# Kernel optimization log

Hardware: AMD Instinct MI355X
Metric: run time of the kernel (lower is better)

Reference implementation:

```python
import jax, jax.numpy as jnp
import numpy as np

D = 384      # embedding_dim
H = 6        # num_heads
HD = D // H  # head_dim = 64
S = 256      # seq_len
B = 64       # batch
EPS = 1e-5


def setup_inputs() -> dict:
    key = jax.random.key(0)
    ks = jax.random.split(key, 16)
    scale = 0.02
    inp = {
        'x': jax.random.normal(ks[0], (B, S, D), dtype=jnp.float32),
        'wq': jax.random.normal(ks[1], (D, D), dtype=jnp.float32) * scale,
        'wk': jax.random.normal(ks[2], (D, D), dtype=jnp.float32) * scale,
        'wv': jax.random.normal(ks[3], (D, D), dtype=jnp.float32) * scale,
        'wo': jax.random.normal(ks[4], (D, D), dtype=jnp.float32) * scale,
        'bo': jnp.zeros((D,), dtype=jnp.float32),
        'w1': jax.random.normal(ks[5], (D, 4 * D), dtype=jnp.float32) * scale,
        'b1': jnp.zeros((4 * D,), dtype=jnp.float32),
        'w2': jax.random.normal(ks[6], (4 * D, D), dtype=jnp.float32) * scale,
        'b2': jnp.zeros((D,), dtype=jnp.float32),
        'g1': jnp.ones((D,), dtype=jnp.float32),
        'be1': jnp.zeros((D,), dtype=jnp.float32),
        'g2': jnp.ones((D,), dtype=jnp.float32),
        'be2': jnp.zeros((D,), dtype=jnp.float32),
    }
    return inp


def _layernorm(x, g, b):
    m = jnp.mean(x, axis=-1, keepdims=True)
    v = jnp.mean((x - m) ** 2, axis=-1, keepdims=True)
    return (x - m) * jax.lax.rsqrt(v + EPS) * g + b


def _block(x, wq, wk, wv, wo, bo, w1, b1, w2, b2, g1, be1, g2, be2):
    b, s, d = x.shape
    h = _layernorm(x, g1, be1)
    # batched per-head projections (equivalent to 6 separate small Linears concatenated)
    q = (h @ wq).reshape(b, s, H, HD).transpose(0, 2, 1, 3)  # [B,H,S,HD]
    k = (h @ wk).reshape(b, s, H, HD).transpose(0, 2, 1, 3)
    v = (h @ wv).reshape(b, s, H, HD).transpose(0, 2, 1, 3)
    scores = jnp.einsum('bhqe,bhke->bhqk', q, k) / np.float32(np.sqrt(HD))
    causal = jnp.tril(jnp.ones((s, s), dtype=bool))
    scores = jnp.where(causal, scores, -jnp.inf)
    attn = jax.nn.softmax(scores, axis=-1)  # dropout = identity in eval
    ctx = jnp.einsum('bhqk,bhke->bhqe', attn, v)  # [B,H,S,HD]
    ctx = ctx.transpose(0, 2, 1, 3).reshape(b, s, d)  # concat heads
    x = x + (ctx @ wo + bo)
    h2 = _layernorm(x, g2, be2)
    ff = jax.nn.relu(h2 @ w1 + b1) @ w2 + b2
    return x + ff


def reference(x, wq, wk, wv, wo, bo, w1, b1, w2, b2, g1, be1, g2, be2):
    return _block(x, wq, wk, wv, wo, bo, w1, b1, w2, b2, g1, be1, g2, be2)
```

## Files before the change

### kernel.cpp

```cpp
#include <hip/hip_runtime.h>
#include <hip/hip_bf16.h>

typedef __hip_bfloat16 bf16;
typedef __attribute__((ext_vector_type(8))) short short8;
typedef __attribute__((ext_vector_type(4))) float f32x4;

#define D_EMB 384
#define NHEAD 6
#define HDIM 64
#define SEQ 256
#define BATCH 64
#define M_ROWS (BATCH * SEQ)
#define DFF (4 * D_EMB)
#define DQKV (3 * D_EMB)

__device__ __forceinline__ void async_load16(const void* gptr, void* lptr) {
    __builtin_amdgcn_global_load_lds(
        (const __attribute__((address_space(1))) unsigned int*)gptr,
        (__attribute__((address_space(3))) unsigned int*)lptr, 16, 0, 0);
}

__global__ __launch_bounds__(256)
void transpose_all(const float* __restrict__ wq, const float* __restrict__ wk,
                   const float* __restrict__ wv, const float* __restrict__ wo,
                   const float* __restrict__ w1, const float* __restrict__ w2,
                   bf16* __restrict__ wqkv_t, bf16* __restrict__ wo_t,
                   bf16* __restrict__ w1_t, bf16* __restrict__ w2_t)
{
    __shared__ float t[32][33];
    const int id = blockIdx.x;
    const float* src; bf16* dst; int K, N, local, nbT;
    if      (id <  144) { src = wq; dst = wqkv_t;               K = 384;  N = 384;  local = id;        nbT = 12; }
    else if (id <  288) { src = wk; dst = wqkv_t + 147456;      K = 384;  N = 384;  local = id - 144;  nbT = 12; }
    else if (id <  432) { src = wv; dst = wqkv_t + 294912;      K = 384;  N = 384;  local = id - 288;  nbT = 12; }
    else if (id <  576) { src = wo; dst = wo_t;                 K = 384;  N = 384;  local = id - 432;  nbT = 12; }
    else if (id < 1152) { src = w1; dst = w1_t;                 K = 384;  N = 1536; local = id - 576;  nbT = 48; }
    else                { src = w2; dst = w2_t;                 K = 1536; N = 384;  local = id - 1152; nbT = 12; }
    const int nb = (local % nbT) * 32, kb = (local / nbT) * 32;
    const int tx = threadIdx.x, ty = threadIdx.y;
#pragma unroll
    for (int i = 0; i < 32; i += 8)
        t[ty + i][tx] = src[(size_t)(kb + ty + i) * N + nb + tx];
    __syncthreads();
#pragma unroll
    for (int i = 0; i < 32; i += 8)
        dst[(size_t)(nb + ty + i) * K + kb + tx] = __float2bfloat16(t[tx][ty + i]);
}

__global__ __launch_bounds__(256)
void ln_kernel(const float* __restrict__ x, const float* __restrict__ g,
               const float* __restrict__ be, bf16* __restrict__ out)
{
    const int row  = blockIdx.x * 4 + (threadIdx.x >> 6);
    const int lane = threadIdx.x & 63;
    const float* xr = x + (size_t)row * D_EMB;

    float v[6];
    float s = 0.f;
#pragma unroll
    for (int i = 0; i < 6; ++i) { v[i] = xr[lane + i * 64]; s += v[i]; }
#pragma unroll
    for (int off = 32; off; off >>= 1) s += __shfl_xor(s, off, 64);
    const float mean = s * (1.f / 384.f);

    float var = 0.f;
#pragma unroll
    for (int i = 0; i < 6; ++i) { float d = v[i] - mean; var += d * d; }
#pragma unroll
    for (int off = 32; off; off >>= 1) var += __shfl_xor(var, off, 64);
    const float rstd = rsqrtf(var * (1.f / 384.f) + 1e-5f);

    bf16* orow = out + (size_t)row * D_EMB;
#pragma unroll
    for (int i = 0; i < 6; ++i) {
        const int c = lane + i * 64;
        orow[c] = __float2bfloat16((v[i] - mean) * rstd * g[c] + be[c]);
    }
}

template<bool RELU, bool OUT_BF16, bool VT>
__global__ __launch_bounds__(256)
void mfma_gemm(const bf16* __restrict__ A, const bf16* __restrict__ Bt,
               const float* __restrict__ bias, const float* __restrict__ res,
               void* __restrict__ Cout, int M, int N, int K, bf16* __restrict__ vt)
{
    __shared__ __attribute__((aligned(16))) unsigned short smem[32768];
    unsigned short* As = smem;
    unsigned short* Bs = smem + 16384;

    const int tid  = threadIdx.x;
    const int wave = tid >> 6;
    const int lane = tid & 63;

    const int nwg = gridDim.x * gridDim.y;
    const int bl  = blockIdx.y * gridDim.x + blockIdx.x;
    const int lb  = (bl & 7) * (nwg >> 3) + (bl >> 3);
    const int m0  = (lb / gridDim.x) * 128;
    const int n0  = (lb % gridDim.x) * 128;

    const int wm = (wave >> 1) * 64;
    const int wn = (wave & 1) * 64;
    const int c16 = lane & 15;
    const int g   = lane >> 4;
    const int lr  = lane >> 3;
    const int ls  = lane & 7;

    f32x4 acc[4][4];
#pragma unroll
    for (int i = 0; i < 4; ++i)
#pragma unroll
        for (int j = 0; j < 4; ++j)
            acc[i][j] = (f32x4){0.f, 0.f, 0.f, 0.f};

    auto stage = [&](int buf, int k0) {
#pragma unroll
        for (int it = 0; it < 4; ++it) {
            const int r = (it * 4 + wave) * 8 + lr;
            const int oct = ls ^ (r & 7);
            async_load16(A + (size_t)(m0 + r) * K + k0 + oct * 8,
                         &As[buf * 8192 + (it * 4 + wave) * 512]);
            async_load16(Bt + (size_t)(n0 + r) * K + k0 + oct * 8,
                         &Bs[buf * 8192 + (it * 4 + wave) * 512]);
        }
    };

    stage(0, 0);
    const int KT = K >> 6;
    for (int kt = 0; kt < KT; ++kt) {
        const int cur = kt & 1;
        __syncthreads();
        if (kt + 1 < KT) stage(cur ^ 1, (kt + 1) * 64);
#pragma unroll
        for (int kk = 0; kk < 2; ++kk) {
            short8 af[4], bfr[4];
#pragma unroll
            for (int i = 0; i < 4; ++i) {
                const int row = wm + i * 16 + c16;
                af[i] = *(const short8*)&As[cur * 8192 + row * 64 + (((kk * 4 + g) ^ (row & 7)) << 3)];
            }
#pragma unroll
            for (int j = 0; j < 4; ++j) {
                const int row = wn + j * 16 + c16;
                bfr[j] = *(const short8*)&Bs[cur * 8192 + row * 64 + (((kk * 4 + g) ^ (row & 7)) << 3)];
            }
#pragma unroll
            for (int i = 0; i < 4; ++i)
#pragma unroll
                for (int j = 0; j < 4; ++j)
                    acc[i][j] = __builtin_amdgcn_mfma_f32_16x16x32_bf16(
                        af[i], bfr[j], acc[i][j], 0, 0, 0);
        }
    }

    const int crow = g * 4;

    if (VT && n0 >= 768) {
        __syncthreads();
        unsigned short* T = smem;
#pragma unroll
        for (int j = 0; j < 4; ++j) {
            const int col = wn + j * 16 + c16;
#pragma unroll
            for (int i = 0; i < 4; ++i)
#pragma unroll
                for (int r = 0; r < 4; ++r) {
                    const int row = wm + i * 16 + crow + r;
                    bf16 pb = __float2bfloat16(acc[i][j][r]);
                    T[col * 128 + ((((row >> 3) ^ (col & 15)) << 3) | (row & 7))] =
                        *(unsigned short*)&pb;
                }
        }
        __syncthreads();
        const int b  = m0 >> 8;
        const int s0 = m0 & 255;
#pragma unroll
        for (int it = 0; it < 8; ++it) {
            const int cc = it * 256 + tid;
            const int col = cc >> 4, o = cc & 15;
            const int gcol = n0 - 768 + col;
            const int h = gcol >> 6, d = gcol & 63;
            const int so = (o ^ (col & 15)) << 3;
            const uint4 v = *(const uint4*)&T[col * 128 + o * 8];
            *(uint4*)(vt + (((size_t)(b * NHEAD + h) * 64 + d) * 256 + s0 + so)) = v;
        }
        return;
    }

    if (OUT_BF16) {
        __syncthreads();
        unsigned short* Cs = smem;
#pragma unroll
        for (int j = 0; j < 4; ++j) {
            const int col = wn + j * 16 + c16;
            const float bv = bias ? bias[n0 + col] : 0.f;
#pragma unroll
            for (int i = 0; i < 4; ++i)
#pragma unroll
                for (int r = 0; r < 4; ++r) {
                    const int row = wm + i * 16 + crow + r;
                    float v = acc[i][j][r] + bv;
                    if (RELU) v = fmaxf(v, 0.f);
                    bf16 pb = __float2bfloat16(v);
                    Cs[row * 128 + ((((col >> 3) ^ (row & 15)) << 3) | (col & 7))] =
                        *(unsigned short*)&pb;
                }
        }
        __syncthreads();
#pragma unroll
        for (int it = 0; it < 8; ++it) {
            const int cc = it * 256 + tid;
            const int row = cc >> 4, o = cc & 15;
            const uint4 v = *(const uint4*)&Cs[row * 128 + ((o ^ (row & 15)) << 3)];
            *(uint4*)((bf16*)Cout + (size_t)(m0 + row) * N + n0 + o * 8) = v;
        }
        return;
    }

#pragma unroll
    for (int j = 0; j < 4; ++j) {
        const int colg = n0 + wn + j * 16 + c16;
        const float bv = bias ? bias[colg] : 0.f;
#pragma unroll
        for (int i = 0; i < 4; ++i) {
            const int rowg = m0 + wm + i * 16 + crow;
#pragma unroll
            for (int r = 0; r < 4; ++r) {
                float v = acc[i][j][r] + bv;
                if (res) v += res[(size_t)(rowg + r) * N + colg];
                if (RELU) v = fmaxf(v, 0.f);
                ((float*)Cout)[(size_t)(rowg + r) * N + colg] = v;
            }
        }
    }
}

template<bool RELU, bool OUT_BF16>
__global__ __launch_bounds__(256)
void mfma_gemm64(const bf16* __restrict__ A, const bf16* __restrict__ Bt,
                 const float* __restrict__ bias, const float* __restrict__ res,
                 void* __restrict__ Cout, int M, int N, int K)
{
    __shared__ __attribute__((aligned(16))) unsigned short smem[24576];
    unsigned short* As = smem;
    unsigned short* Bs = smem + 8192;

    const int tid  = threadIdx.x;
    const int wave = tid >> 6;
    const int lane = tid & 63;

    const int nwg = gridDim.x * gridDim.y;
    const int bl  = blockIdx.y * gridDim.x + blockIdx.x;
    const int lb  = (bl & 7) * (nwg >> 3) + (bl >> 3);
    const int m0  = (lb / gridDim.x) * 64;
    const int n0  = (lb % gridDim.x) * 128;

    const int wm = (wave >> 1) * 32;
    const int wn = (wave & 1) * 64;
    const int c16 = lane & 15;
    const int g   = lane >> 4;
    const int lr  = lane >> 3;
    const int ls  = lane & 7;

    f32x4 acc[2][4];
#pragma unroll
    for (int i = 0; i < 2; ++i)
#pragma unroll
        for (int j = 0; j < 4; ++j)
            acc[i][j] = (f32x4){0.f, 0.f, 0.f, 0.f};

    auto stage = [&](int buf, int k0) {
#pragma unroll
        for (int it = 0; it < 2; ++it) {
            const int r = (it * 4 + wave) * 8 + lr;
            const int oct = ls ^ (r & 7);
            async_load16(A + (size_t)(m0 + r) * K + k0 + oct * 8,
                         &As[buf * 4096 + (it * 4 + wave) * 512]);
        }
#pragma unroll
        for (int it = 0; it < 4; ++it) {
            const int r = (it * 4 + wave) * 8 + lr;
            const int oct = ls ^ (r & 7);
            async_load16(Bt + (size_t)(n0 + r) * K + k0 + oct * 8,
                         &Bs[buf * 8192 + (it * 4 + wave) * 512]);
        }
    };

    stage(0, 0);
    const int KT = K >> 6;
    for (int kt = 0; kt < KT; ++kt) {
        const int cur = kt & 1;
        __syncthreads();
        if (kt + 1 < KT) stage(cur ^ 1, (kt + 1) * 64);
#pragma unroll
        for (int kk = 0; kk < 2; ++kk) {
            short8 af[2], bfr[4];
#pragma unroll
            for (int i = 0; i < 2; ++i) {
                const int row = wm + i * 16 + c16;
                af[i] = *(const short8*)&As[cur * 4096 + row * 64 + (((kk * 4 + g) ^ (row & 7)) << 3)];
            }
#pragma unroll
            for (int j = 0; j < 4; ++j) {
                const int row = wn + j * 16 + c16;
                bfr[j] = *(const short8*)&Bs[cur * 8192 + row * 64 + (((kk * 4 + g) ^ (row & 7)) << 3)];
            }
#pragma unroll
            for (int i = 0; i < 2; ++i)
#pragma unroll
                for (int j = 0; j < 4; ++j)
                    acc[i][j] = __builtin_amdgcn_mfma_f32_16x16x32_bf16(
                        af[i], bfr[j], acc[i][j], 0, 0, 0);
        }
    }

    const int crow = g * 4;

    if (OUT_BF16) {
        __syncthreads();
        unsigned short* Cs = smem;
#pragma unroll
        for (int j = 0; j < 4; ++j) {
            const int col = wn + j * 16 + c16;
            const float bv = bias ? bias[n0 + col] : 0.f;
#pragma unroll
            for (int i = 0; i < 2; ++i)
#pragma unroll
                for (int r = 0; r < 4; ++r) {
                    const int row = wm + i * 16 + crow + r;
                    float v = acc[i][j][r] + bv;
                    if (RELU) v = fmaxf(v, 0.f);
                    bf16 pb = __float2bfloat16(v);
                    Cs[row * 128 + ((((col >> 3) ^ (row & 15)) << 3) | (col & 7))] =
                        *(unsigned short*)&pb;
                }
        }
        __syncthreads();
#pragma unroll
        for (int it = 0; it < 4; ++it) {
            const int cc = it * 256 + tid;
            const int row = cc >> 4, o = cc & 15;
            const uint4 v = *(const uint4*)&Cs[row * 128 + ((o ^ (row & 15)) << 3)];
            *(uint4*)((bf16*)Cout + (size_t)(m0 + row) * N + n0 + o * 8) = v;
        }
        return;
    }

#pragma unroll
    for (int j = 0; j < 4; ++j) {
        const int colg = n0 + wn + j * 16 + c16;
        const float bv = bias ? bias[colg] : 0.f;
#pragma unroll
        for (int i = 0; i < 2; ++i) {
            const int rowg = m0 + wm + i * 16 + crow;
#pragma unroll
            for (int r = 0; r < 4; ++r) {
                float v = acc[i][j][r] + bv;
                if (res) v += res[(size_t)(rowg + r) * N + colg];
                if (RELU) v = fmaxf(v, 0.f);
                ((float*)Cout)[(size_t)(rowg + r) * N + colg] = v;
            }
        }
    }
}

#define ATT_SCALE 0.18033688f

__global__ __launch_bounds__(64, 2)
void attn_mfma(const bf16* __restrict__ qkv, const bf16* __restrict__ vt,
               bf16* __restrict__ ctx)
{
    __shared__ __attribute__((aligned(16))) unsigned short bufKP[4096];
    __shared__ __attribute__((aligned(16))) unsigned short bufV[4096];

    const int nb   = gridDim.x;
    const int bid0 = blockIdx.x;
    const int bid  = (bid0 & 7) * (nb >> 3) + (bid0 >> 3);
    const int bh = bid >> 2, qi = bid & 3;
    const int b = bh / NHEAD, h = bh % NHEAD;
    const int lane = threadIdx.x;
    const int g = lane >> 4;
    const int c = lane & 15;
    const int lr = lane >> 3;
    const int ls = lane & 7;

    const size_t qbase  = (size_t)b * SEQ * DQKV + (size_t)h * HDIM;
    const size_t vtbase = (size_t)bh * HDIM * SEQ;

    short8 qf[4][2];
#pragma unroll
    for (int i = 0; i < 4; ++i)
#pragma unroll
        for (int kf = 0; kf < 2; ++kf)
            qf[i][kf] = *(const short8*)(qkv + qbase +
                (size_t)(qi * 64 + i * 16 + c) * DQKV + kf * 32 + g * 8);

    short8 ones;
#pragma unroll
    for (int e = 0; e < 8; ++e) ones[e] = (short)0x3F80;

    f32x4 acc_o[4][4], acc_l[4];
#pragma unroll
    for (int i = 0; i < 4; ++i) {
        acc_l[i] = (f32x4){0.f, 0.f, 0.f, 0.f};
#pragma unroll
        for (int n = 0; n < 4; ++n)
            acc_o[i][n] = (f32x4){0.f, 0.f, 0.f, 0.f};
    }

    for (int jt = 0; jt <= qi; ++jt) {
#pragma unroll
        for (int it = 0; it < 8; ++it) {
            const int row = it * 8 + lr;
            const int oct = ls ^ (row & 7);
            async_load16(qkv + qbase + (size_t)(jt * 64 + row) * DQKV + D_EMB + oct * 8,
                         bufKP + it * 512);
            async_load16(vt + vtbase + (size_t)row * SEQ + jt * 64 + oct * 8,
                         bufV + it * 512);
        }
        asm volatile("s_waitcnt vmcnt(0)" ::: "memory");

        short8 kb[2][4];
#pragma unroll
        for (int kf = 0; kf < 2; ++kf)
#pragma unroll
            for (int j = 0; j < 4; ++j) {
                const int row = j * 16 + c;
                kb[kf][j] = *(const short8*)&bufKP[row * 64 + (((kf * 4 + g) ^ (row & 7)) << 3)];
            }

        const bool diag = (jt == qi);
#pragma unroll
        for (int i = 0; i < 4; ++i) {
            f32x4 s[4];
#pragma unroll
            for (int j = 0; j < 4; ++j) s[j] = (f32x4){0.f, 0.f, 0.f, 0.f};
#pragma unroll
            for (int kf = 0; kf < 2; ++kf)
#pragma unroll
                for (int j = 0; j < 4; ++j)
                    s[j] = __builtin_amdgcn_mfma_f32_16x16x32_bf16(
                        qf[i][kf], kb[kf][j], s[j], 0, 0, 0);

#pragma unroll
            for (int r = 0; r < 4; ++r) {
                const int row = i * 16 + g * 4 + r;
#pragma unroll
                for (int j = 0; j < 4; ++j) {
                    const int col = j * 16 + c;
                    float p = exp2f(s[j][r] * ATT_SCALE);
                    if (diag && col > row) p = 0.f;
                    bf16 pb = __float2bfloat16(p);
                    bufKP[row * 64 + (((col >> 3) ^ (row & 7)) << 3) + (col & 7)] =
                        *(unsigned short*)&pb;
                }
            }
        }

#pragma unroll
        for (int kf = 0; kf < 2; ++kf) {
            short8 pa[4], vb[4];
#pragma unroll
            for (int i = 0; i < 4; ++i) {
                const int row = i * 16 + c;
                pa[i] = *(const short8*)&bufKP[row * 64 + (((kf * 4 + g) ^ (row & 7)) << 3)];
            }
#pragma unroll
            for (int n = 0; n < 4; ++n) {
                const int row = n * 16 + c;
                vb[n] = *(const short8*)&bufV[row * 64 + (((kf * 4 + g) ^ (row & 7)) << 3)];
            }
#pragma unroll
            for (int i = 0; i < 4; ++i) {
#pragma unroll
                for (int n = 0; n < 4; ++n)
                    acc_o[i][n] = __builtin_amdgcn_mfma_f32_16x16x32_bf16(
                        pa[i], vb[n], acc_o[i][n], 0, 0, 0);
                acc_l[i] = __builtin_amdgcn_mfma_f32_16x16x32_bf16(
                    pa[i], ones, acc_l[i], 0, 0, 0);
            }
        }
    }

    const size_t obase = (size_t)b * SEQ * D_EMB + (size_t)h * HDIM;
#pragma unroll
    for (int i = 0; i < 4; ++i)
#pragma unroll
        for (int r = 0; r < 4; ++r) {
            const float rl = 1.f / acc_l[i][r];
            const int row = qi * 64 + i * 16 + g * 4 + r;
#pragma unroll
            for (int n = 0; n < 4; ++n) {
                const int col = n * 16 + c;
                ctx[obase + (size_t)row * D_EMB + col] =
                    __float2bfloat16(acc_o[i][n][r] * rl);
            }
        }
}

extern "C" void kernel_launch(void* const* d_in, const int* in_sizes, int n_in,
                              void* d_out, int out_size, void* d_ws, size_t ws_size,
                              hipStream_t stream)
{
    const float* x  = (const float*)d_in[0];
    const float* wq = (const float*)d_in[1];
    const float* wk = (const float*)d_in[2];
    const float* wv = (const float*)d_in[3];
    const float* wo = (const float*)d_in[4];
    const float* bo = (const float*)d_in[5];
    const float* w1 = (const float*)d_in[6];
    const float* b1 = (const float*)d_in[7];
    const float* w2 = (const float*)d_in[8];
    const float* b2 = (const float*)d_in[9];
    const float* g1  = (const float*)d_in[10];
    const float* be1 = (const float*)d_in[11];
    const float* g2  = (const float*)d_in[12];
    const float* be2 = (const float*)d_in[13];
    float* out = (float*)d_out;
    (void)in_sizes; (void)n_in; (void)out_size; (void)ws_size;

    char* w = (char*)d_ws;
    bf16* wqkv_t = (bf16*)(w);
    bf16* wo_t   = (bf16*)(w + (size_t)(1024 * 1024));
    bf16* w1_t   = (bf16*)(w + (size_t)(1536 * 1024));
    bf16* w2_t   = (bf16*)(w + (size_t)(2816 * 1024));
    char* slotA  = w + 4 * 1024 * 1024;
    char* slotB  = slotA + (size_t)M_ROWS * D_EMB * sizeof(bf16);

    bf16* h1  = (bf16*)slotA;
    bf16* ctx = (bf16*)slotA;
    bf16* h2  = (bf16*)slotA;
    bf16* qkv = (bf16*)slotB;
    bf16* vt  = (bf16*)slotB + (size_t)M_ROWS * DQKV;
    bf16* ff1 = (bf16*)slotB;

    const dim3 blk(256);

    transpose_all<<<dim3(1728), dim3(32, 8), 0, stream>>>(
        wq, wk, wv, wo, w1, w2, wqkv_t, wo_t, w1_t, w2_t);

    ln_kernel<<<dim3(M_ROWS / 4), blk, 0, stream>>>(x, g1, be1, h1);

    mfma_gemm<false, true, true><<<dim3(DQKV / 128, M_ROWS / 128), blk, 0, stream>>>(
        h1, wqkv_t, nullptr, nullptr, qkv, M_ROWS, DQKV, D_EMB, vt);

    attn_mfma<<<dim3(BATCH * NHEAD * 4), dim3(64), 0, stream>>>(qkv, vt, ctx);

    mfma_gemm64<false, false><<<dim3(D_EMB / 128, M_ROWS / 64), blk, 0, stream>>>(
        ctx, wo_t, bo, x, out, M_ROWS, D_EMB, D_EMB);

    ln_kernel<<<dim3(M_ROWS / 4), blk, 0, stream>>>(out, g2, be2, h2);

    mfma_gemm64<true, true><<<dim3(DFF / 128, M_ROWS / 64), blk, 0, stream>>>(
        h2, w1_t, b1, nullptr, ff1, M_ROWS, DFF, D_EMB);

    mfma_gemm64<false, false><<<dim3(D_EMB / 128, M_ROWS / 64), blk, 0, stream>>>(
        ff1, w2_t, b2, out, out, M_ROWS, D_EMB, DFF);
}
```

Measured before the change: 241.8 us.

## Fuse output projection GEMM with residual add and second LayerNorm

Replaces the separate O-projection GEMM and LN2 kernel with a single kernel in which each workgroup computes a full 64x384 row tile. LayerNorm statistics are reduced across lanes and waves in the epilogue, and the normalized bf16 output is written directly. This removes one launch and the re-read of the fp32 residual output by the LN kernel. In exchange it uses a large LDS footprint (about 112KB), holds 96 accumulator floats per thread with fewer workgroups, and computes variance with the one-pass E[x^2]-mean^2 formula.

Result: faster. 233.1 us (-3.6%).

```diff
diff --git a/kernel.cpp b/kernel.cpp
--- a/kernel.cpp
+++ b/kernel.cpp
@@ -361,6 +361,153 @@
             }
         }
     }
+}
+
+__global__ __launch_bounds__(256)
+void oproj_ln(const bf16* __restrict__ A, const bf16* __restrict__ Bt,
+              const float* __restrict__ bo, const float* __restrict__ x,
+              const float* __restrict__ g2, const float* __restrict__ be2,
+              float* __restrict__ out, bf16* __restrict__ h2)
+{
+    __shared__ __attribute__((aligned(16))) unsigned short smem[57344];
+    unsigned short* As = smem;
+    unsigned short* Bs = smem + 8192;
+    __shared__ float lnred[64][4];
+
+    const int tid  = threadIdx.x;
+    const int wave = tid >> 6;
+    const int lane = tid & 63;
+
+    const int nwg = gridDim.x;
+    const int bl  = blockIdx.x;
+    const int lb  = (bl & 7) * (nwg >> 3) + (bl >> 3);
+    const int m0  = lb * 64;
+
+    const int wm  = (wave >> 1) * 32;
+    const int wn  = (wave & 1) * 192;
+    const int c16 = lane & 15;
+    const int g   = lane >> 4;
+    const int lr  = lane >> 3;
+    const int ls  = lane & 7;
+
+    f32x4 acc[2][12];
+#pragma unroll
+    for (int i = 0; i < 2; ++i)
+#pragma unroll
+        for (int j = 0; j < 12; ++j)
+            acc[i][j] = (f32x4){0.f, 0.f, 0.f, 0.f};
+
+    auto stage = [&](int buf, int k0) {
+#pragma unroll
+        for (int it = 0; it < 2; ++it) {
+            const int r = (it * 4 + wave) * 8 + lr;
+            const int oct = ls ^ (r & 7);
+            async_load16(A + (size_t)(m0 + r) * D_EMB + k0 + oct * 8,
+                         &As[buf * 4096 + (it * 4 + wave) * 512]);
+        }
+#pragma unroll
+        for (int it = 0; it < 12; ++it) {
+            const int r = (it * 4 + wave) * 8 + lr;
+            const int oct = ls ^ (r & 7);
+            async_load16(Bt + (size_t)r * D_EMB + k0 + oct * 8,
+                         &Bs[buf * 24576 + (it * 4 + wave) * 512]);
+        }
+    };
+
+    stage(0, 0);
+    const int KT = D_EMB >> 6;
+    for (int kt = 0; kt < KT; ++kt) {
+        const int cur = kt & 1;
+        __syncthreads();
+        if (kt + 1 < KT) stage(cur ^ 1, (kt + 1) * 64);
+#pragma unroll
+        for (int kk = 0; kk < 2; ++kk) {
+            short8 af[2], bfr[12];
+#pragma unroll
+            for (int i = 0; i < 2; ++i) {
+                const int row = wm + i * 16 + c16;
+                af[i] = *(const short8*)&As[cur * 4096 + row * 64 + (((kk * 4 + g) ^ (row & 7)) << 3)];
+            }
+#pragma unroll
+            for (int j = 0; j < 12; ++j) {
+                const int row = wn + j * 16 + c16;
+                bfr[j] = *(const short8*)&Bs[cur * 24576 + row * 64 + (((kk * 4 + g) ^ (row & 7)) << 3)];
+            }
+#pragma unroll
+            for (int i = 0; i < 2; ++i)
+#pragma unroll
+                for (int j = 0; j < 12; ++j)
+                    acc[i][j] = __builtin_amdgcn_mfma_f32_16x16x32_bf16(
+                        af[i], bfr[j], acc[i][j], 0, 0, 0);
+        }
+    }
+
+    const int crow = g * 4;
+    float rsum[2][4], rsq[2][4];
+#pragma unroll
+    for (int i = 0; i < 2; ++i)
+#pragma unroll
+        for (int r = 0; r < 4; ++r) { rsum[i][r] = 0.f; rsq[i][r] = 0.f; }
+
+#pragma unroll
+    for (int j = 0; j < 12; ++j) {
+        const int col = wn + j * 16 + c16;
+        const float bv = bo[col];
+#pragma unroll
+        for (int i = 0; i < 2; ++i) {
+            const int rowg = m0 + wm + i * 16 + crow;
+#pragma unroll
+            for (int r = 0; r < 4; ++r) {
+                float v = acc[i][j][r] + bv + x[(size_t)(rowg + r) * D_EMB + col];
+                acc[i][j][r] = v;
+                out[(size_t)(rowg + r) * D_EMB + col] = v;
+                rsum[i][r] += v;
+                rsq[i][r]  += v * v;
+            }
+        }
+    }
+
+#pragma unroll
+    for (int off = 8; off; off >>= 1) {
+#pragma unroll
+        for (int i = 0; i < 2; ++i)
+#pragma unroll
+            for (int r = 0; r < 4; ++r) {
+                rsum[i][r] += __shfl_xor(rsum[i][r], off, 64);
+                rsq[i][r]  += __shfl_xor(rsq[i][r], off, 64);
+            }
+    }
+    const int half = (wave & 1) * 2;
+    if (c16 == 0) {
+#pragma unroll
+        for (int i = 0; i < 2; ++i)
+#pragma unroll
+            for (int r = 0; r < 4; ++r) {
+                const int row = wm + i * 16 + crow + r;
+                lnred[row][half + 0] = rsum[i][r];
+                lnred[row][half + 1] = rsq[i][r];
+            }
+    }
+    __syncthreads();
+
+#pragma unroll
+    for (int i = 0; i < 2; ++i)
+#pragma unroll
+        for (int r = 0; r < 4; ++r) {
+            const int row  = wm + i * 16 + crow + r;
+            const float s  = lnred[row][0] + lnred[row][2];
+            const float q  = lnred[row][1] + lnred[row][3];
+            const float mean = s * (1.f / 384.f);
+            const float var  = q * (1.f / 384.f) - mean * mean;
+            const float rstd = rsqrtf(var + 1e-5f);
+            const size_t rb = (size_t)(m0 + row) * D_EMB;
+#pragma unroll
+            for (int j = 0; j < 12; ++j) {
+                const int col = wn + j * 16 + c16;
+                h2[rb + col] = __float2bfloat16(
+                    (acc[i][j][r] - mean) * rstd * g2[col] + be2[col]);
+            }
+        }
 }
 
 #define ATT_SCALE 0.18033688f
@@ -545,10 +692,8 @@
 
     attn_mfma<<<dim3(BATCH * NHEAD * 4), dim3(64), 0, stream>>>(qkv, vt, ctx);
 
-    mfma_gemm64<false, false><<<dim3(D_EMB / 128, M_ROWS / 64), blk, 0, stream>>>(
-        ctx, wo_t, bo, x, out, M_ROWS, D_EMB, D_EMB);
-
-    ln_kernel<<<dim3(M_ROWS / 4), blk, 0, stream>>>(out, g2, be2, h2);
+    oproj_ln<<<dim3(M_ROWS / 64), blk, 0, stream>>>(
+        ctx, wo_t, bo, x, g2, be2, out, h2);
 
     mfma_gemm64<true, true><<<dim3(DFF / 128, M_ROWS / 64), blk, 0, stream>>>(
         h2, w1_t, b1, nullptr, ff1, M_ROWS, DFF, D_EMB);
```
